# Kernel optimization log

Hardware: AMD Instinct MI355X
Metric: run time of the kernel (lower is better)

The kernel has to match this reference:

```python
import jax, jax.numpy as jnp
import numpy as np

NUM_HEADS = 16
D_MODEL = 1024
HEAD_DIM = D_MODEL // NUM_HEADS
EMB = 1024
B, L = 2, 2048


def setup_inputs() -> dict:
    key = jax.random.key(0)
    k1, k2, k3 = jax.random.split(key, 3)
    scale_in = 1.0 / np.sqrt(EMB)
    scale_out = 1.0 / np.sqrt(D_MODEL)
    return {
        "x": jax.random.normal(k1, (B, L, EMB), dtype=jnp.float32),
        "W_qkv": jax.random.normal(k2, (EMB, 3 * D_MODEL), dtype=jnp.float32) * scale_in,
        "b_qkv": jnp.zeros((3 * D_MODEL,), dtype=jnp.float32),
        "W_out": jax.random.normal(k3, (D_MODEL, EMB), dtype=jnp.float32) * scale_out,
        "b_out": jnp.zeros((EMB,), dtype=jnp.float32),
    }


def reference(x, W_qkv, b_qkv, W_out, b_out):
    Bn, Ln, _ = x.shape
    qkv = x @ W_qkv + b_qkv  # [B, L, 3*d_model]
    q = qkv[:, :, :D_MODEL].reshape(Bn, Ln, NUM_HEADS, HEAD_DIM)
    k = qkv[:, :, D_MODEL:2 * D_MODEL].reshape(Bn, Ln, NUM_HEADS, HEAD_DIM)
    v = qkv[:, :, 2 * D_MODEL:].reshape(Bn, Ln, NUM_HEADS, HEAD_DIM)
    scores = jnp.einsum('bqhd,bkhd->bhqk', q, k)  # [B, H, L, L]
    attn = jax.nn.softmax(scores / jnp.sqrt(jnp.float32(HEAD_DIM)), axis=-1)
    out = jnp.einsum('bhqk,bkhd->bqhd', attn, v).reshape(Bn, Ln, D_MODEL)
    return out @ W_out + b_out
```

## Files before the change

### kernel.cpp

```cpp
#include <hip/hip_runtime.h>
#include <stdint.h>

#define B_   2
#define L_   2048
#define H_   16
#define D_   64
#define EMB_ 1024
#define DM_  1024
#define N3_  3072
#define TOK_ 4096

typedef unsigned short u16;
typedef unsigned int u32;
typedef __attribute__((ext_vector_type(4))) float f32x4;
typedef __attribute__((ext_vector_type(8))) short s16x8;
typedef __attribute__((ext_vector_type(2))) u32 u32x2;
typedef __attribute__((ext_vector_type(4))) u16 u16x4;

#define MFMA(a,b,c) __builtin_amdgcn_mfma_f32_16x16x32_bf16(a,b,c,0,0,0)

#define AS1 __attribute__((address_space(1)))
#define AS3 __attribute__((address_space(3)))
#define GLLDS(g, l) __builtin_amdgcn_global_load_lds( \
    (const AS1 u32*)(const void*)(g), (AS3 u32*)(void*)(l), 16, 0, 0)

#define QSCALE 0.18033688011f

static __device__ __forceinline__ u16 f2bf(float f) {
  u32 u = __builtin_bit_cast(u32, f);
  return (u16)((u + 0x8000u) >> 16);
}

static __device__ __forceinline__ float bf2f(u16 v) {
  u32 u = ((u32)v) << 16;
  return __builtin_bit_cast(float, u);
}

static __device__ __forceinline__ u16 f2h(float f) {
  _Float16 h = (_Float16)f;
  return __builtin_bit_cast(u16, h);
}

static __device__ __forceinline__ float h2f(u16 v) {
  _Float16 h = __builtin_bit_cast(_Float16, v);
  return (float)h;
}

static __device__ __forceinline__ u32 pack2bf(float a, float b) {
  u32 ua = __builtin_bit_cast(u32, a) + 0x8000u;
  u32 ub = __builtin_bit_cast(u32, b) + 0x8000u;
  return __builtin_amdgcn_perm(ub, ua, 0x07060302u);
}

static __device__ __forceinline__ float fexp2(float x) {
#if __has_builtin(__builtin_amdgcn_exp2f)
  return __builtin_amdgcn_exp2f(x);
#else
  float r;
  asm("v_exp_f32 %0, %1" : "=v"(r) : "v"(x));
  return r;
#endif
}

__global__ __launch_bounds__(256) void k_prep(
    const float* __restrict__ x,   u16* __restrict__ xb,
    const float* __restrict__ Wq,  u16* __restrict__ wqT,
    const float* __restrict__ Wo,  u16* __restrict__ woT)
{
  const int blk = blockIdx.x, tid = threadIdx.x;
  if (blk < 4096) {
    int i = (blk * 256 + tid) * 4;
    float4 v = *(const float4*)(x + i);
    ushort4 o;
    o.x = f2bf(v.x); o.y = f2bf(v.y); o.z = f2bf(v.z); o.w = f2bf(v.w);
    *(ushort4*)(xb + i) = o;
    return;
  }
  __shared__ float tile[32][33];
  const float* in;
  u16* out;
  int R, C, bx, by;
  if (blk < 4096 + 3072) {
    int t = blk - 4096;
    in = Wq; out = wqT; R = EMB_; C = N3_;
    bx = t % 96; by = t / 96;
  } else {
    int t = blk - 7168;
    in = Wo; out = woT; R = DM_; C = DM_;
    bx = t & 31; by = t >> 5;
  }
  int c0 = bx * 32, r0 = by * 32;
  int tx = tid & 31, ty = tid >> 5;
  #pragma unroll
  for (int i = 0; i < 32; i += 8)
    tile[ty + i][tx] = in[(size_t)(r0 + ty + i) * C + (c0 + tx)];
  __syncthreads();
  int c = tid >> 3, j = tid & 7;
  u16x4 o;
  #pragma unroll
  for (int r = 0; r < 4; ++r)
    o[r] = f2bf(tile[j * 4 + r][c]);
  *(u16x4*)(out + (size_t)(c0 + c) * R + r0 + j * 4) = o;
}

template<int EPI, int BN>
__global__ __launch_bounds__(256, 4) void k_gemm(
    const u16* __restrict__ A, const u16* __restrict__ Bt,
    const float* __restrict__ bias, int M, int N, int K,
    float* __restrict__ Cf,
    u16* __restrict__ Qo, u16* __restrict__ Ko, u16* __restrict__ Vo)
{
  constexpr int NF = BN / 32;
  constexpr int BROWS = (BN == 128) ? 32 : 16;
  const int tid = threadIdx.x;
  const int wave = tid >> 6, lane = tid & 63;
  const int lr = lane & 15, lk = lane >> 4;
  const int wr = wave >> 1, wc = wave & 1;
  const int m0 = blockIdx.y * 128, n0 = blockIdx.x * BN;

  __shared__ u16 As[2][128 * 32];
  __shared__ u16 Bs[2][BN * 32];

  f32x4 acc[4][NF] = {};

  const int srow = wave * 32 + (lane >> 2);
  const int srowB = (BN == 128) ? srow : (wave * 16 + (lane >> 2));
  const int schunk = (lane & 3) * 8;
  const u16* gA = A  + (size_t)(m0 + srow) * K + schunk;
  const u16* gB = Bt + (size_t)(n0 + srowB) * K + schunk;
  const size_t rstep = (size_t)16 * K;
  u16* lA0 = (u16*)As[0] + wave * (32 * 32);
  u16* lA1 = (u16*)As[1] + wave * (32 * 32);
  u16* lB0 = (u16*)Bs[0] + wave * (BROWS * 32);
  u16* lB1 = (u16*)Bs[1] + wave * (BROWS * 32);

  GLLDS(gA,         lA0);
  GLLDS(gA + rstep, lA0 + 16 * 32);
  GLLDS(gB,         lB0);
  if (BN == 128) GLLDS(gB + rstep, lB0 + 16 * 32);

  int buf = 0;
  for (int k0 = 0; k0 < K; k0 += 32, buf ^= 1) {
    __syncthreads();

    if (k0 + 32 < K) {
      u16* dA = buf ? lA0 : lA1;
      u16* dB = buf ? lB0 : lB1;
      GLLDS(gA + k0 + 32,         dA);
      GLLDS(gA + k0 + 32 + rstep, dA + 16 * 32);
      GLLDS(gB + k0 + 32,         dB);
      if (BN == 128) GLLDS(gB + k0 + 32 + rstep, dB + 16 * 32);
    }

    const u16* Ab = (const u16*)As[buf];
    const u16* Bb = (const u16*)Bs[buf];
    s16x8 af[4], bfr[NF];
    #pragma unroll
    for (int mi = 0; mi < 4; ++mi)
      af[mi] = *(const s16x8*)(Ab + (wr * 64 + mi * 16 + lr) * 32 + lk * 8);
    #pragma unroll
    for (int ni = 0; ni < NF; ++ni)
      bfr[ni] = *(const s16x8*)(Bb + (wc * (BN / 2) + ni * 16 + lr) * 32 + lk * 8);
    #pragma unroll
    for (int mi = 0; mi < 4; ++mi)
      #pragma unroll
      for (int ni = 0; ni < NF; ++ni)
        acc[mi][ni] = MFMA(af[mi], bfr[ni], acc[mi][ni]);
  }

  const int mbase = m0 + wr * 64 + lk * 4;
  #pragma unroll
  for (int ni = 0; ni < NF; ++ni) {
    int gn = n0 + wc * (BN / 2) + ni * 16 + lr;
    float bz = bias[gn];
    if (EPI == 1) {
      #pragma unroll
      for (int mi = 0; mi < 4; ++mi)
        #pragma unroll
        for (int r = 0; r < 4; ++r) {
          int gm = mbase + mi * 16 + r;
          Cf[(size_t)gm * N + gn] = acc[mi][ni][r] + bz;
        }
    } else {
      int sec = gn >> 10, cm = gn & 1023;
      int h = cm >> 6, d = cm & 63;
      if (sec == 2) {
        #pragma unroll
        for (int mi = 0; mi < 4; ++mi) {
          int gm0 = mbase + mi * 16;
          int b = gm0 >> 11, l0 = gm0 & 2047;
          int bh = b * H_ + h;
          u16x4 vv;
          #pragma unroll
          for (int r = 0; r < 4; ++r) vv[r] = f2bf(acc[mi][ni][r] + bz);
          *(u16x4*)(Vo + ((size_t)bh * D_ + d) * L_ + l0) = vv;
        }
      } else {
        #pragma unroll
        for (int mi = 0; mi < 4; ++mi)
          #pragma unroll
          for (int r = 0; r < 4; ++r) {
            int gm = mbase + mi * 16 + r;
            float v = acc[mi][ni][r] + bz;
            int b = gm >> 11, l = gm & 2047;
            int bh = b * H_ + h;
            if (sec == 0) Qo[((size_t)bh * L_ + l) * D_ + d] = f2bf(v * QSCALE);
            else          Ko[((size_t)bh * L_ + l) * D_ + d] = f2bf(v);
          }
      }
    }
  }
}

__global__ __launch_bounds__(256, 2) void k_flash(
    const u16* __restrict__ Q, const u16* __restrict__ Kb,
    const u16* __restrict__ Vt,
    u16* __restrict__ O0, u16* __restrict__ O1, float* __restrict__ lpart)
{
  const int tid = threadIdx.x;
  const int wave = tid >> 6, lane = tid & 63;
  const int lr = lane & 15, lk = lane >> 4;
  const int blk = blockIdx.x;
  const int idx = blk >> 3;
  const int bh = (blk & 7) * 4 + (idx >> 4);
  const int rem = idx & 15;
  const int qt = rem >> 1;
  const int half = rem & 1;
  const int tbase = half * 1024;
  const int b = bh >> 4, h = bh & 15;
  const u16* Qh = Q  + (size_t)bh * L_ * D_;
  const u16* Kh = Kb + (size_t)bh * L_ * D_;
  const u16* Vh = Vt + (size_t)bh * D_ * L_;

  __shared__ u16 Ks[2][64 * 64];
  __shared__ u16 Vs[2][64 * 64];
  __shared__ u16 Ps[256 * 64];

  const int qrow0 = qt * 256 + wave * 64;
  s16x8 qf[4][2];
  #pragma unroll
  for (int g = 0; g < 4; ++g)
    #pragma unroll
    for (int ks = 0; ks < 2; ++ks)
      qf[g][ks] = *(const s16x8*)(Qh + (size_t)(qrow0 + g * 16 + lr) * D_ + ks * 32 + lk * 8);

  f32x4 acco[4][4] = {};
  float lst[4] = {0.f, 0.f, 0.f, 0.f};

  const int srow0 = wave * 16 + (lane >> 3);
  const int gch8 = (((lane & 7) ^ ((lane >> 3) & 7)) * 8);
  u16* kd0 = (u16*)Ks[0] + wave * (16 * 64);
  u16* kd1 = (u16*)Ks[1] + wave * (16 * 64);
  u16* vd0 = (u16*)Vs[0] + wave * (16 * 64);
  u16* vd1 = (u16*)Vs[1] + wave * (16 * 64);

  const int ck0 = (lk ^ (lr & 7)) * 8;
  const int sxor = (lr & 7) << 1;
  u16* PsW = Ps + wave * (64 * 64);

  GLLDS(Kh + (size_t)(tbase + srow0) * 64 + gch8,       kd0);
  GLLDS(Kh + (size_t)(tbase + srow0 + 8) * 64 + gch8,   kd0 + 8 * 64);
  GLLDS(Vh + ((size_t)srow0 * L_ + tbase + gch8),       vd0);
  GLLDS(Vh + ((size_t)(srow0 + 8) * L_ + tbase + gch8), vd0 + 8 * 64);

  int buf = 0;
  for (int t0 = tbase; t0 < tbase + 1024; t0 += 64, buf ^= 1) {
    __syncthreads();

    if (t0 + 64 < tbase + 1024) {
      const int tn = t0 + 64;
      u16* kd = buf ? kd0 : kd1;
      u16* vd = buf ? vd0 : vd1;
      GLLDS(Kh + (size_t)(tn + srow0) * 64 + gch8,       kd);
      GLLDS(Kh + (size_t)(tn + srow0 + 8) * 64 + gch8,   kd + 8 * 64);
      GLLDS(Vh + ((size_t)srow0 * L_ + tn + gch8),       vd);
      GLLDS(Vh + ((size_t)(srow0 + 8) * L_ + tn + gch8), vd + 8 * 64);
    }

    const u16* Kbuf = (const u16*)Ks[buf];
    f32x4 accs[4][4] = {};
    s16x8 kf[4][2];
    #pragma unroll
    for (int mi = 0; mi < 4; ++mi) {
      const u16* rp = Kbuf + (mi * 16 + lr) * 64;
      kf[mi][0] = *(const s16x8*)(rp + ck0);
      kf[mi][1] = *(const s16x8*)(rp + (ck0 ^ 32));
    }
    #pragma unroll
    for (int mi = 0; mi < 4; ++mi)
      #pragma unroll
      for (int g = 0; g < 4; ++g) {
        accs[g][mi] = MFMA(kf[mi][0], qf[g][0], accs[g][mi]);
        accs[g][mi] = MFMA(kf[mi][1], qf[g][1], accs[g][mi]);
      }

    #pragma unroll
    for (int g = 0; g < 4; ++g) {
      const int prow = (g * 16 + lr) * 64;
      #pragma unroll
      for (int mi = 0; mi < 4; ++mi) {
        float p0 = fexp2(accs[g][mi][0]);
        float p1 = fexp2(accs[g][mi][1]);
        float p2 = fexp2(accs[g][mi][2]);
        float p3 = fexp2(accs[g][mi][3]);
        lst[g] += (p0 + p1) + (p2 + p3);
        u32x2 pk = { pack2bf(p0, p1), pack2bf(p2, p3) };
        *(u32x2*)(PsW + prow + (((4 * mi + lk) ^ sxor) * 4)) = pk;
      }
    }

    const u16* Vbuf = (const u16*)Vs[buf];
    s16x8 vf[4][2], pf[4][2];
    #pragma unroll
    for (int di = 0; di < 4; ++di) {
      const u16* rp = Vbuf + (di * 16 + lr) * 64;
      vf[di][0] = *(const s16x8*)(rp + ck0);
      vf[di][1] = *(const s16x8*)(rp + (ck0 ^ 32));
    }
    #pragma unroll
    for (int g = 0; g < 4; ++g) {
      const int prow = (g * 16 + lr) * 64;
      pf[g][0] = *(const s16x8*)(PsW + prow + (((2 * lk) ^ sxor) * 4));
      pf[g][1] = *(const s16x8*)(PsW + prow + (((8 + 2 * lk) ^ sxor) * 4));
    }
    #pragma unroll
    for (int di = 0; di < 4; ++di)
      #pragma unroll
      for (int g = 0; g < 4; ++g) {
        acco[g][di] = MFMA(vf[di][0], pf[g][0], acco[g][di]);
        acco[g][di] = MFMA(vf[di][1], pf[g][1], acco[g][di]);
      }
  }

  u16* Oh = half ? O1 : O0;
  #pragma unroll
  for (int g = 0; g < 4; ++g) {
    float l = lst[g];
    l += __shfl_xor(l, 16);
    l += __shfl_xor(l, 32);
    const int q = qrow0 + g * 16 + lr;
    if (lk == 0)
      lpart[((size_t)(half << 5) + bh) * L_ + q] = l;
    #pragma unroll
    for (int di = 0; di < 4; ++di) {
      u16x4 o;
      #pragma unroll
      for (int r = 0; r < 4; ++r)
        o[r] = f2h(acco[g][di][r]);
      *(u16x4*)(Oh + (size_t)(b * L_ + q) * DM_ + h * D_ + di * 16 + lk * 4) = o;
    }
  }
}

__global__ __launch_bounds__(256) void k_comb(
    const u16* __restrict__ O0, const u16* __restrict__ O1,
    const float* __restrict__ lpart, u16* __restrict__ AO)
{
  const int row = blockIdx.x;
  const int b = row >> 11, l = row & 2047;
  const int c = threadIdx.x * 4;
  const int h = c >> 6;
  const size_t bhl = (size_t)(b * H_ + h) * L_ + l;
  const float rl = 1.0f / (lpart[bhl] + lpart[(size_t)32 * L_ + bhl]);
  const size_t off = (size_t)row * DM_ + c;
  u16x4 a = *(const u16x4*)(O0 + off);
  u16x4 bb = *(const u16x4*)(O1 + off);
  u16x4 o;
  #pragma unroll
  for (int r = 0; r < 4; ++r)
    o[r] = f2bf((h2f(a[r]) + h2f(bb[r])) * rl);
  *(u16x4*)(AO + off) = o;
}

extern "C" void kernel_launch(void* const* d_in, const int* in_sizes, int n_in,
                              void* d_out, int out_size, void* d_ws, size_t ws_size,
                              hipStream_t stream)
{
  const float* x    = (const float*)d_in[0];
  const float* Wqkv = (const float*)d_in[1];
  const float* bqkv = (const float*)d_in[2];
  const float* Wout = (const float*)d_in[3];
  const float* bout = (const float*)d_in[4];
  float* out = (float*)d_out;

  u16* xb  = (u16*)d_ws;
  u16* wqT = xb  + (size_t)TOK_ * EMB_;
  u16* woT = wqT + (size_t)N3_ * EMB_;
  u16* qb  = woT + (size_t)DM_ * EMB_;
  u16* kb  = qb  + (size_t)B_ * H_ * L_ * D_;
  u16* vt  = kb  + (size_t)B_ * H_ * L_ * D_;
  u16* ao  = vt  + (size_t)B_ * H_ * L_ * D_;
  float* lpart = (float*)wqT;

  k_prep<<<4096 + 3072 + 1024, 256, 0, stream>>>(x, xb, Wqkv, wqT, Wout, woT);
  k_gemm<0, 128><<<dim3(N3_ / 128, TOK_ / 128), 256, 0, stream>>>(
      xb, wqT, bqkv, TOK_, N3_, EMB_, nullptr, qb, kb, vt);
  k_flash<<<512, 256, 0, stream>>>(qb, kb, vt, ao, xb, lpart);
  k_comb<<<TOK_, 256, 0, stream>>>(ao, xb, lpart, ao);
  k_gemm<1, 64><<<dim3(DM_ / 64, TOK_ / 128), 256, 0, stream>>>(
      ao, woT, bout, TOK_, DM_, EMB_, out, nullptr, nullptr, nullptr);
}
```

Before: 185.2 us.

## Fuse partial-output combine into output projection GEMM A-tile loading

Removes the separate combine kernel that summed the two half-sequence partial attention outputs and normalised them by the softmax denominators. The output-projection GEMM now loads both fp16 partials and the denominators straight into registers. It combines and converts them to bf16, then writes the A tile to shared memory after the MFMAs, so the loads overlap compute. This saves one launch and a full write and re-read of the combined activation. In exchange, A-tile loads move from async global-to-LDS to register-staged loads, partial traffic per tile doubles across the column blocks, and the launch-bounds occupancy hint for this GEMM drops to 2.

Measured after the change: 197.1 us. 1.06x slower.

```diff
diff --git a/kernel.cpp b/kernel.cpp
--- a/kernel.cpp
+++ b/kernel.cpp
@@ -104,11 +104,13 @@
 }
 
 template<int EPI, int BN>
-__global__ __launch_bounds__(256, 4) void k_gemm(
+__global__ __launch_bounds__(256, (EPI == 1) ? 2 : 4) void k_gemm(
     const u16* __restrict__ A, const u16* __restrict__ Bt,
     const float* __restrict__ bias, int M, int N, int K,
     float* __restrict__ Cf,
-    u16* __restrict__ Qo, u16* __restrict__ Ko, u16* __restrict__ Vo)
+    u16* __restrict__ Qo, u16* __restrict__ Ko, u16* __restrict__ Vo,
+    const u16* __restrict__ P0, const u16* __restrict__ P1,
+    const float* __restrict__ lp)
 {
   constexpr int NF = BN / 32;
   constexpr int BROWS = (BN == 128) ? 32 : 16;
@@ -126,7 +128,8 @@
   const int srow = wave * 32 + (lane >> 2);
   const int srowB = (BN == 128) ? srow : (wave * 16 + (lane >> 2));
   const int schunk = (lane & 3) * 8;
-  const u16* gA = A  + (size_t)(m0 + srow) * K + schunk;
+  const u16* Abase = (EPI == 1) ? Bt : A;
+  const u16* gA = Abase + (size_t)(m0 + srow) * K + schunk;
   const u16* gB = Bt + (size_t)(n0 + srowB) * K + schunk;
   const size_t rstep = (size_t)16 * K;
   u16* lA0 = (u16*)As[0] + wave * (32 * 32);
@@ -134,8 +137,30 @@
   u16* lB0 = (u16*)Bs[0] + wave * (BROWS * 32);
   u16* lB1 = (u16*)Bs[1] + wave * (BROWS * 32);
 
-  GLLDS(gA,         lA0);
-  GLLDS(gA + rstep, lA0 + 16 * 32);
+  const int arow0 = m0 + srow;
+  const int ab0 = (arow0 >> 11), al0 = arow0 & 2047;
+  const int ab1 = ((arow0 + 16) >> 11), al1 = (arow0 + 16) & 2047;
+
+  if constexpr (EPI == 1) {
+    #pragma unroll
+    for (int s = 0; s < 2; ++s) {
+      const int row = arow0 + s * 16;
+      const size_t aoff = (size_t)row * 1024 + schunk;
+      s16x8 o0 = *(const s16x8*)(P0 + aoff);
+      s16x8 o1 = *(const s16x8*)(P1 + aoff);
+      const int bb = s ? ab1 : ab0, ll = s ? al1 : al0;
+      const size_t bhl = (size_t)(bb * H_ + (schunk >> 6)) * L_ + ll;
+      const float rl = 1.0f / (lp[bhl] + lp[(size_t)32 * L_ + bhl]);
+      s16x8 w;
+      #pragma unroll
+      for (int j = 0; j < 8; ++j)
+        w[j] = (short)f2bf((h2f((u16)o0[j]) + h2f((u16)o1[j])) * rl);
+      *(s16x8*)(lA0 + s * (16 * 32) + lane * 8) = w;
+    }
+  } else {
+    GLLDS(gA,         lA0);
+    GLLDS(gA + rstep, lA0 + 16 * 32);
+  }
   GLLDS(gB,         lB0);
   if (BN == 128) GLLDS(gB + rstep, lB0 + 16 * 32);
 
@@ -143,13 +168,31 @@
   for (int k0 = 0; k0 < K; k0 += 32, buf ^= 1) {
     __syncthreads();
 
-    if (k0 + 32 < K) {
-      u16* dA = buf ? lA0 : lA1;
+    const bool stage = (k0 + 32 < K);
+    s16x8 p0a, p1a, p0b, p1b;
+    float rla, rlb;
+    if (stage) {
       u16* dB = buf ? lB0 : lB1;
-      GLLDS(gA + k0 + 32,         dA);
-      GLLDS(gA + k0 + 32 + rstep, dA + 16 * 32);
-      GLLDS(gB + k0 + 32,         dB);
+      GLLDS(gB + k0 + 32, dB);
       if (BN == 128) GLLDS(gB + k0 + 32 + rstep, dB + 16 * 32);
+      if constexpr (EPI == 1) {
+        const int k0n = k0 + 32;
+        const int h = (k0n + schunk) >> 6;
+        const size_t a0 = (size_t)arow0 * 1024 + k0n + schunk;
+        p0a = *(const s16x8*)(P0 + a0);
+        p1a = *(const s16x8*)(P1 + a0);
+        const size_t a1 = a0 + (size_t)16 * 1024;
+        p0b = *(const s16x8*)(P0 + a1);
+        p1b = *(const s16x8*)(P1 + a1);
+        const size_t bhl0 = (size_t)(ab0 * H_ + h) * L_ + al0;
+        const size_t bhl1 = (size_t)(ab1 * H_ + h) * L_ + al1;
+        rla = 1.0f / (lp[bhl0] + lp[(size_t)32 * L_ + bhl0]);
+        rlb = 1.0f / (lp[bhl1] + lp[(size_t)32 * L_ + bhl1]);
+      } else {
+        u16* dA = buf ? lA0 : lA1;
+        GLLDS(gA + k0 + 32,         dA);
+        GLLDS(gA + k0 + 32 + rstep, dA + 16 * 32);
+      }
     }
 
     const u16* Ab = (const u16*)As[buf];
@@ -166,6 +209,20 @@
       #pragma unroll
       for (int ni = 0; ni < NF; ++ni)
         acc[mi][ni] = MFMA(af[mi], bfr[ni], acc[mi][ni]);
+
+    if constexpr (EPI == 1) {
+      if (stage) {
+        u16* dA = buf ? lA0 : lA1;
+        s16x8 w0, w1;
+        #pragma unroll
+        for (int j = 0; j < 8; ++j) {
+          w0[j] = (short)f2bf((h2f((u16)p0a[j]) + h2f((u16)p1a[j])) * rla);
+          w1[j] = (short)f2bf((h2f((u16)p0b[j]) + h2f((u16)p1b[j])) * rlb);
+        }
+        *(s16x8*)(dA + lane * 8) = w0;
+        *(s16x8*)(dA + 16 * 32 + lane * 8) = w1;
+      }
+    }
   }
 
   const int mbase = m0 + wr * 64 + lk * 4;
@@ -352,26 +409,6 @@
   }
 }
 
-__global__ __launch_bounds__(256) void k_comb(
-    const u16* __restrict__ O0, const u16* __restrict__ O1,
-    const float* __restrict__ lpart, u16* __restrict__ AO)
-{
-  const int row = blockIdx.x;
-  const int b = row >> 11, l = row & 2047;
-  const int c = threadIdx.x * 4;
-  const int h = c >> 6;
-  const size_t bhl = (size_t)(b * H_ + h) * L_ + l;
-  const float rl = 1.0f / (lpart[bhl] + lpart[(size_t)32 * L_ + bhl]);
-  const size_t off = (size_t)row * DM_ + c;
-  u16x4 a = *(const u16x4*)(O0 + off);
-  u16x4 bb = *(const u16x4*)(O1 + off);
-  u16x4 o;
-  #pragma unroll
-  for (int r = 0; r < 4; ++r)
-    o[r] = f2bf((h2f(a[r]) + h2f(bb[r])) * rl);
-  *(u16x4*)(AO + off) = o;
-}
-
 extern "C" void kernel_launch(void* const* d_in, const int* in_sizes, int n_in,
                               void* d_out, int out_size, void* d_ws, size_t ws_size,
                               hipStream_t stream)
@@ -394,9 +431,10 @@
 
   k_prep<<<4096 + 3072 + 1024, 256, 0, stream>>>(x, xb, Wqkv, wqT, Wout, woT);
   k_gemm<0, 128><<<dim3(N3_ / 128, TOK_ / 128), 256, 0, stream>>>(
-      xb, wqT, bqkv, TOK_, N3_, EMB_, nullptr, qb, kb, vt);
+      xb, wqT, bqkv, TOK_, N3_, EMB_, nullptr, qb, kb, vt,
+      nullptr, nullptr, nullptr);
   k_flash<<<512, 256, 0, stream>>>(qb, kb, vt, ao, xb, lpart);
-  k_comb<<<TOK_, 256, 0, stream>>>(ao, xb, lpart, ao);
   k_gemm<1, 64><<<dim3(DM_ / 64, TOK_ / 128), 256, 0, stream>>>(
-      ao, woT, bout, TOK_, DM_, EMB_, out, nullptr, nullptr, nullptr);
-}
+      nullptr, woT, bout, TOK_, DM_, EMB_, out, nullptr, nullptr, nullptr,
+      ao, xb, lpart);
+}
```

## Add dedicated output-projection GEMM and pad P tile stride in flash kernel

Applied to the files above, without the earlier changes.

Replaces the templated output GEMM with a specialised k_gemm1 that has compile-time sizes, 4-blocks-per-CU launch bounds, a 2x2 wave layout and swizzled double-buffered LDS loads. It also pads the per-wave P scratch row stride in the flash kernel from 64 to 68 elements, aiming to reduce LDS bank conflicts. The padding raises LDS use in k_flash slightly, and the padded stride combined with the existing XOR swizzle may break 16-byte alignment of the P reads.

Result: slower. 206.6 us (+11.5%).

```diff
diff --git a/kernel.cpp b/kernel.cpp
--- a/kernel.cpp
+++ b/kernel.cpp
@@ -212,6 +212,87 @@
   }
 }
 
+__global__ __launch_bounds__(256, 4) void k_gemm1(
+    const u16* __restrict__ A, const u16* __restrict__ Bt,
+    const float* __restrict__ bias, float* __restrict__ Cf)
+{
+  const int tid = threadIdx.x;
+  const int wave = tid >> 6, lane = tid & 63;
+  const int lr = lane & 15, lk = lane >> 4;
+  const int wr = wave >> 1, wc = wave & 1;
+  const int m0 = blockIdx.y * 128, n0 = blockIdx.x * 64;
+  const int K = EMB_, N = DM_;
+
+  __shared__ u16 As[2][128 * 64];
+  __shared__ u16 Bs[2][64 * 64];
+
+  f32x4 acc[4][2] = {};
+
+  const int srow8 = lane >> 3;
+  const int gch8 = (((lane & 7) ^ srow8) * 8);
+  const u16* gA = A  + (size_t)(m0 + wave * 32 + srow8) * K + gch8;
+  const u16* gB = Bt + (size_t)(n0 + wave * 16 + srow8) * K + gch8;
+  const size_t r8 = (size_t)8 * K;
+  u16* lA0 = (u16*)As[0] + wave * (32 * 64);
+  u16* lA1 = (u16*)As[1] + wave * (32 * 64);
+  u16* lB0 = (u16*)Bs[0] + wave * (16 * 64);
+  u16* lB1 = (u16*)Bs[1] + wave * (16 * 64);
+
+  #pragma unroll
+  for (int i = 0; i < 4; ++i) GLLDS(gA + i * r8, lA0 + i * (8 * 64));
+  #pragma unroll
+  for (int i = 0; i < 2; ++i) GLLDS(gB + i * r8, lB0 + i * (8 * 64));
+
+  const int cx = lr & 7;
+  int buf = 0;
+  for (int k0 = 0; k0 < K; k0 += 64, buf ^= 1) {
+    __syncthreads();
+
+    if (k0 + 64 < K) {
+      u16* dA = buf ? lA0 : lA1;
+      u16* dB = buf ? lB0 : lB1;
+      #pragma unroll
+      for (int i = 0; i < 4; ++i) GLLDS(gA + k0 + 64 + i * r8, dA + i * (8 * 64));
+      #pragma unroll
+      for (int i = 0; i < 2; ++i) GLLDS(gB + k0 + 64 + i * r8, dB + i * (8 * 64));
+    }
+
+    const u16* Ab = (const u16*)As[buf];
+    const u16* Bb = (const u16*)Bs[buf];
+    #pragma unroll
+    for (int ksub = 0; ksub < 2; ++ksub) {
+      const int ch = ((ksub * 4 + lk) ^ cx) * 8;
+      s16x8 af[4], bfr[2];
+      #pragma unroll
+      for (int mi = 0; mi < 4; ++mi)
+        af[mi] = *(const s16x8*)(Ab + (wr * 64 + mi * 16 + lr) * 64 + ch);
+      #pragma unroll
+      for (int ni = 0; ni < 2; ++ni)
+        bfr[ni] = *(const s16x8*)(Bb + (wc * 32 + ni * 16 + lr) * 64 + ch);
+      #pragma unroll
+      for (int mi = 0; mi < 4; ++mi)
+        #pragma unroll
+        for (int ni = 0; ni < 2; ++ni)
+          acc[mi][ni] = MFMA(af[mi], bfr[ni], acc[mi][ni]);
+    }
+  }
+
+  const int mbase = m0 + wr * 64 + lk * 4;
+  #pragma unroll
+  for (int ni = 0; ni < 2; ++ni) {
+    int gn = n0 + wc * 32 + ni * 16 + lr;
+    float bz = bias[gn];
+    #pragma unroll
+    for (int mi = 0; mi < 4; ++mi)
+      #pragma unroll
+      for (int r = 0; r < 4; ++r) {
+        int gm = mbase + mi * 16 + r;
+        Cf[(size_t)gm * N + gn] = acc[mi][ni][r] + bz;
+      }
+  }
+}
+
+#define PSTR 68
 __global__ __launch_bounds__(256, 2) void k_flash(
     const u16* __restrict__ Q, const u16* __restrict__ Kb,
     const u16* __restrict__ Vt,
@@ -234,7 +315,7 @@
 
   __shared__ u16 Ks[2][64 * 64];
   __shared__ u16 Vs[2][64 * 64];
-  __shared__ u16 Ps[256 * 64];
+  __shared__ u16 Ps[256 * PSTR];
 
   const int qrow0 = qt * 256 + wave * 64;
   s16x8 qf[4][2];
@@ -256,7 +337,7 @@
 
   const int ck0 = (lk ^ (lr & 7)) * 8;
   const int sxor = (lr & 7) << 1;
-  u16* PsW = Ps + wave * (64 * 64);
+  u16* PsW = Ps + wave * (64 * PSTR);
 
   GLLDS(Kh + (size_t)(tbase + srow0) * 64 + gch8,       kd0);
   GLLDS(Kh + (size_t)(tbase + srow0 + 8) * 64 + gch8,   kd0 + 8 * 64);
@@ -296,7 +377,7 @@
 
     #pragma unroll
     for (int g = 0; g < 4; ++g) {
-      const int prow = (g * 16 + lr) * 64;
+      const int prow = (g * 16 + lr) * PSTR;
       #pragma unroll
       for (int mi = 0; mi < 4; ++mi) {
         float p0 = fexp2(accs[g][mi][0]);
@@ -319,7 +400,7 @@
     }
     #pragma unroll
     for (int g = 0; g < 4; ++g) {
-      const int prow = (g * 16 + lr) * 64;
+      const int prow = (g * 16 + lr) * PSTR;
       pf[g][0] = *(const s16x8*)(PsW + prow + (((2 * lk) ^ sxor) * 4));
       pf[g][1] = *(const s16x8*)(PsW + prow + (((8 + 2 * lk) ^ sxor) * 4));
     }
@@ -397,6 +478,5 @@
       xb, wqT, bqkv, TOK_, N3_, EMB_, nullptr, qb, kb, vt);
   k_flash<<<512, 256, 0, stream>>>(qb, kb, vt, ao, xb, lpart);
   k_comb<<<TOK_, 256, 0, stream>>>(ao, xb, lpart, ao);
-  k_gemm<1, 64><<<dim3(DM_ / 64, TOK_ / 128), 256, 0, stream>>>(
-      ao, woT, bout, TOK_, DM_, EMB_, out, nullptr, nullptr, nullptr);
-}
+  k_gemm1<<<dim3(DM_ / 64, TOK_ / 128), 256, 0, stream>>>(ao, woT, bout, out);
+}
```
